# Performance work log

Measured on AMD Instinct MI355X. Metric: run time of the kernel, lower is better.

The kernel has to match this reference:

```python
import jax, jax.numpy as jnp
import numpy as np

D = 256        # feature dim
H = 8          # num_heads
HD = D // H    # head dim = 32
G = 16         # graphs in batch
NA = 128       # nodes per graph, side A
NB = 128       # nodes per graph, side B


def setup_inputs() -> dict:
    key = jax.random.key(0)
    ks = jax.random.split(key, 7)
    s = 1.0 / np.sqrt(D)
    A = jax.random.normal(ks[0], (G * NA, D), dtype=jnp.float32)
    B = jax.random.normal(ks[1], (G * NB, D), dtype=jnp.float32)
    batch1 = jnp.repeat(jnp.arange(G, dtype=jnp.int64), NA)
    batch2 = jnp.repeat(jnp.arange(G, dtype=jnp.int64), NB)
    W1 = jax.random.normal(ks[2], (D, D), dtype=jnp.float32) * s
    bias1 = jax.random.normal(ks[3], (D,), dtype=jnp.float32) * s
    W2 = jax.random.normal(ks[4], (D, D), dtype=jnp.float32) * s
    bias2 = jax.random.normal(ks[5], (D,), dtype=jnp.float32) * s
    q = jax.random.normal(ks[6], (HD,), dtype=jnp.float32) * s
    return {"A": A, "batch1": batch1, "B": B, "batch2": batch2,
            "W1": W1, "bias1": bias1, "W2": W2, "bias2": bias2, "q": q}


def reference(A, batch1, B, batch2, W1, bias1, W2, bias2, q):
    # equal-size graphs: counts are uniform, so torch.split == reshape
    g = int(np.asarray(batch1)[-1]) + 1
    nA = A.shape[0] // g
    nB = B.shape[0] // g
    x1 = A @ W1.T + bias1            # [g*nA, D]
    x2 = B @ W2.T + bias2            # [g*nB, D]
    # faithful to torch: raw C-order view [nA, D] -> [H, nA, HD]
    x1 = x1.reshape(g, H, nA, HD)    # [g, H, nA, hd]
    x2 = x2.reshape(g, H, nB, HD)    # [g, H, nB, hd]
    # att[g,h,i,j] = sum_k tanh(x1[g,h,i,k] * x2[g,h,j,k]) * q[k]
    att = jnp.einsum('ghijk,k->ghij',
                     jnp.tanh(x1[:, :, :, None, :] * x2[:, :, None, :, :]), q)
    b2a = jax.nn.softmax(att.mean(axis=3), axis=2)   # [g, H, nA]
    a2b = jax.nn.softmax(att.mean(axis=2), axis=2)   # [g, H, nB]
    A_p = jnp.einsum('ghik,ghi->ghk', x1, b2a).reshape(g, D)
    B_p = jnp.einsum('ghjk,ghj->ghk', x2, a2b).reshape(g, D)
    return jnp.concatenate([A_p, B_p], axis=1)       # [g, 2D]
```

## Files before the change

### kernel.cpp

```cpp
#include <hip/hip_runtime.h>

#define C2L2E 2.8853900817779268f
#define LOG2E 1.4426950408889634f

#define WS_X1   0
#define WS_X2   524288
#define WS_RS   1048576
#define WS_CQ   1064960

typedef short bf16x8 __attribute__((ext_vector_type(8)));
typedef float f32x4 __attribute__((ext_vector_type(4)));

__device__ __forceinline__ unsigned short bf16rne(float f) {
    unsigned u = __float_as_uint(f);
    u += 0x7FFF + ((u >> 16) & 1);
    return (unsigned short)(u >> 16);
}
__device__ __forceinline__ float bf16tof(unsigned short h) {
    return __uint_as_float(((unsigned)h) << 16);
}
__device__ __forceinline__ float rfl(float x) {
    return __uint_as_float(__builtin_amdgcn_readfirstlane(__float_as_uint(x)));
}
__device__ __forceinline__ void cvt4(float4 v, ushort4* h, ushort4* l) {
    h->x = bf16rne(v.x); l->x = bf16rne(v.x - bf16tof(h->x));
    h->y = bf16rne(v.y); l->y = bf16rne(v.y - bf16tof(h->y));
    h->z = bf16rne(v.z); l->z = bf16rne(v.z - bf16tof(h->z));
    h->w = bf16rne(v.w); l->w = bf16rne(v.w - bf16tof(h->w));
}

__global__ __launch_bounds__(512) void k01_gemm(
        const float* __restrict__ A, const float* __restrict__ B,
        const float* __restrict__ W1, const float* __restrict__ b1,
        const float* __restrict__ W2, const float* __restrict__ b2,
        float* __restrict__ ws) {
    __shared__ unsigned short AH[2048], AL[2048], WH[2048], WL[2048];
    const int bid = blockIdx.x, tid = threadIdx.x;
    const int mat = bid >> 7, idx = bid & 127;
    const int r0 = (idx >> 2) * 64, c0 = (idx & 3) * 64;
    const float* In = mat ? B : A;
    const float* Wm = mat ? W2 : W1;
    const float* bs = mat ? b2 : b1;
    float* xo = ws + (mat ? WS_X2 : WS_X1);

    const int wv = tid >> 6, lane = tid & 63;
    const int rt = wv & 3;
    const int nt0 = (wv >> 2) * 2;

    const int lr = tid >> 3, k4 = tid & 7;
    const int wofs = (((lr >> 4) * 64 + (lr & 15) + ((k4 >> 1) << 4)) * 8 + (k4 & 1) * 4);

    f32x4 acc[2];
    acc[0] = (f32x4){0.f, 0.f, 0.f, 0.f};
    acc[1] = (f32x4){0.f, 0.f, 0.f, 0.f};

    for (int kt = 0; kt < 8; ++kt) {
        if (kt) __syncthreads();
        {
            float4 va = *(const float4*)(In + (size_t)(r0 + lr) * 256 + kt * 32 + k4 * 4);
            ushort4 h, l; cvt4(va, &h, &l);
            *(ushort4*)(AH + wofs) = h;
            *(ushort4*)(AL + wofs) = l;
            float4 vw = *(const float4*)(Wm + (size_t)(c0 + lr) * 256 + kt * 32 + k4 * 4);
            cvt4(vw, &h, &l);
            *(ushort4*)(WH + wofs) = h;
            *(ushort4*)(WL + wofs) = l;
        }
        __syncthreads();
        {
            bf16x8 ah = *(const bf16x8*)(AH + (rt * 64 + lane) * 8);
            bf16x8 al = *(const bf16x8*)(AL + (rt * 64 + lane) * 8);
            #pragma unroll
            for (int nt = 0; nt < 2; ++nt) {
                const int ct = nt0 + nt;
                bf16x8 wh = *(const bf16x8*)(WH + (ct * 64 + lane) * 8);
                bf16x8 wl = *(const bf16x8*)(WL + (ct * 64 + lane) * 8);
                acc[nt] = __builtin_amdgcn_mfma_f32_16x16x32_bf16(ah, wh, acc[nt], 0, 0, 0);
                acc[nt] = __builtin_amdgcn_mfma_f32_16x16x32_bf16(ah, wl, acc[nt], 0, 0, 0);
                acc[nt] = __builtin_amdgcn_mfma_f32_16x16x32_bf16(al, wh, acc[nt], 0, 0, 0);
            }
        }
    }

    const int rowb = r0 + rt * 16 + (lane >> 4) * 4;
    const int l16 = lane & 15;
    #pragma unroll
    for (int nt = 0; nt < 2; ++nt) {
        const int col = c0 + (nt0 + nt) * 16 + l16;
        const float bb = bs[col];
        #pragma unroll
        for (int rg = 0; rg < 4; ++rg)
            xo[(size_t)(rowb + rg) * 256 + col] = acc[nt][rg] + bb;
    }
}

__global__ __launch_bounds__(512, 6) void k2_att(
        const float* __restrict__ x1v, const float* __restrict__ x2v,
        const float* __restrict__ q,
        float* __restrict__ rowsum, float* __restrict__ colq) {
    const int bid = blockIdx.x;
    const int gh = bid >> 2;
    const int qd = bid & 3;
    const int tid = threadIdx.x;
    const int j = tid & 127;
    const int iset = __builtin_amdgcn_readfirstlane(tid >> 7);

    __shared__ float Smat[32 * 132];
    __shared__ float colp[4][128];
    __shared__ float red8[32][8];

    float xr[32];
    {
        const float4* xp = (const float4*)(x2v + (size_t)gh * 4096 + (size_t)j * 32);
        #pragma unroll
        for (int k4 = 0; k4 < 8; ++k4) {
            float4 v = xp[k4];
            xr[k4*4+0] = v.x * C2L2E; xr[k4*4+1] = v.y * C2L2E;
            xr[k4*4+2] = v.z * C2L2E; xr[k4*4+3] = v.w * C2L2E;
        }
    }
    float qt[32];
    #pragma unroll
    for (int k4 = 0; k4 < 8; ++k4) {
        float4 v = *(const float4*)(q + k4 * 4);
        qt[k4*4+0] = rfl(v.x) * -2.0f;
        qt[k4*4+1] = rfl(v.y) * -2.0f;
        qt[k4*4+2] = rfl(v.z) * -2.0f;
        qt[k4*4+3] = rfl(v.w) * -2.0f;
    }

    const float* x1base = x1v + (size_t)gh * 4096 + (size_t)(qd * 32 + iset * 8) * 32;
    float colacc = 0.f;

    for (int r = 0; r < 8; ++r) {
        float a[32];
        #pragma unroll
        for (int k4 = 0; k4 < 8; ++k4) {
            float4 v = *(const float4*)(x1base + r * 32 + k4 * 4);
            a[k4*4+0] = rfl(v.x);
            a[k4*4+1] = rfl(v.y);
            a[k4*4+2] = rfl(v.z);
            a[k4*4+3] = rfl(v.w);
        }
        float S0 = 0.f, S1 = 0.f;
        #pragma unroll
        for (int kp = 0; kp < 16; ++kp) {
            float p0 = a[2*kp]   * xr[2*kp];
            float p1 = a[2*kp+1] * xr[2*kp+1];
            float d0 = __builtin_amdgcn_exp2f(fminf(p0, 60.f)) + 1.f;
            float d1 = __builtin_amdgcn_exp2f(fminf(p1, 60.f)) + 1.f;
            float rD = __builtin_amdgcn_rcpf(d0 * d1);
            float U  = fmaf(qt[2*kp+1], d0, qt[2*kp] * d1);
            if (kp & 1) S1 = fmaf(U, rD, S1); else S0 = fmaf(U, rD, S0);
        }
        float S = S0 + S1;
        colacc += S;
        Smat[(iset * 8 + r) * 132 + j] = S;
    }
    colp[iset][j] = colacc;
    __syncthreads();

    if (tid < 256) {
        const int row = tid >> 3, seg = tid & 7;
        const float4* sp = (const float4*)(Smat + row * 132 + seg * 16);
        float4 v0 = sp[0], v1 = sp[1], v2 = sp[2], v3 = sp[3];
        red8[row][seg] = (v0.x+v0.y+v0.z+v0.w) + (v1.x+v1.y+v1.z+v1.w)
                       + (v2.x+v2.y+v2.z+v2.w) + (v3.x+v3.y+v3.z+v3.w);
    }
    __syncthreads();
    if (tid < 32) {
        float s = 0.f;
        #pragma unroll
        for (int m = 0; m < 8; ++m) s += red8[tid][m];
        rowsum[gh * 128 + qd * 32 + tid] = s;
    }
    if (tid < 128) {
        colq[(size_t)bid * 128 + tid] =
            colp[0][tid] + colp[1][tid] + colp[2][tid] + colp[3][tid];
    }
}

__global__ __launch_bounds__(256) void k3_out(
        const float* __restrict__ x1v, const float* __restrict__ x2v,
        const float* __restrict__ rowsum, const float* __restrict__ colq,
        float* __restrict__ out) {
    const int gh = blockIdx.x;
    const int g = gh >> 3, h = gh & 7;
    const int tid = threadIdx.x;
    const int side = tid >> 7;
    const int u = tid & 127;
    const int w2 = (u >> 6) & 1;
    const int lane = tid & 63;

    __shared__ float warr[2][128];
    __shared__ float red[4];
    __shared__ float red2[4];
    __shared__ float part[2][4][32];

    float m;
    if (side == 0) {
        m = rowsum[gh * 128 + u] * 0.0078125f;
    } else {
        m = (colq[(size_t)(gh * 4 + 0) * 128 + u] + colq[(size_t)(gh * 4 + 1) * 128 + u] +
             colq[(size_t)(gh * 4 + 2) * 128 + u] + colq[(size_t)(gh * 4 + 3) * 128 + u]) * 0.0078125f;
    }

    float mx = m;
    #pragma unroll
    for (int s = 32; s >= 1; s >>= 1) mx = fmaxf(mx, __shfl_xor(mx, s));
    if (lane == 0) red[side * 2 + w2] = mx;
    __syncthreads();
    mx = fmaxf(red[side * 2], red[side * 2 + 1]);

    float e = __builtin_amdgcn_exp2f((m - mx) * LOG2E);
    float sm = e;
    #pragma unroll
    for (int s = 32; s >= 1; s >>= 1) sm += __shfl_xor(sm, s);
    if (lane == 0) red2[side * 2 + w2] = sm;
    __syncthreads();
    const float tot = red2[side * 2] + red2[side * 2 + 1];
    warr[side][u] = e * __builtin_amdgcn_rcpf(tot);
    __syncthreads();

    const int k = u & 31, is = u >> 5;
    const float* xt = (side ? x2v : x1v) + (size_t)gh * 4096;
    float p = 0.f;
    #pragma unroll 4
    for (int r = 0; r < 32; ++r)
        p = fmaf(xt[(is * 32 + r) * 32 + k], warr[side][is * 32 + r], p);
    part[side][is][k] = p;
    __syncthreads();
    if (u < 32) {
        float o = part[side][0][u] + part[side][1][u] + part[side][2][u] + part[side][3][u];
        out[(size_t)g * 512 + side * 256 + h * 32 + u] = o;
    }
}

extern "C" void kernel_launch(void* const* d_in, const int* in_sizes, int n_in,
                              void* d_out, int out_size, void* d_ws, size_t ws_size,
                              hipStream_t stream) {
    const float* A  = (const float*)d_in[0];
    const float* B  = (const float*)d_in[2];
    const float* W1 = (const float*)d_in[4];
    const float* b1 = (const float*)d_in[5];
    const float* W2 = (const float*)d_in[6];
    const float* b2 = (const float*)d_in[7];
    const float* q  = (const float*)d_in[8];
    float* ws  = (float*)d_ws;
    float* out = (float*)d_out;

    k01_gemm<<<256, 512, 0, stream>>>(A, B, W1, b1, W2, b2, ws);
    k2_att<<<512, 512, 0, stream>>>(ws + WS_X1, ws + WS_X2, q, ws + WS_RS, ws + WS_CQ);
    k3_out<<<128, 256, 0, stream>>>(ws + WS_X1, ws + WS_X2, ws + WS_RS, ws + WS_CQ, out);
}
```

Before: 37.45 us.

## Fuse softmax/output stage into attention kernel via last-block atomic ticket

Removes the separate k3_out launch. Each (graph, head) group of four attention blocks increments an atomic counter after writing its partial row and column sums, and the last block to arrive computes both softmaxes and the weighted output. The counter is zeroed inside the GEMM kernel. This saves one kernel launch and its dependency gap, at the cost of thread fences, an atomic per block, and extra shared memory in the attention kernel, which may lower occupancy.

```diff
diff --git a/kernel.cpp b/kernel.cpp
--- a/kernel.cpp
+++ b/kernel.cpp
@@ -7,6 +7,7 @@
 #define WS_X2   524288
 #define WS_RS   1048576
 #define WS_CQ   1064960
+#define WS_CNT  1130496
 
 typedef short bf16x8 __attribute__((ext_vector_type(8)));
 typedef float f32x4 __attribute__((ext_vector_type(4)));
@@ -33,9 +34,10 @@
         const float* __restrict__ A, const float* __restrict__ B,
         const float* __restrict__ W1, const float* __restrict__ b1,
         const float* __restrict__ W2, const float* __restrict__ b2,
-        float* __restrict__ ws) {
+        float* __restrict__ ws, int* __restrict__ cnt) {
     __shared__ unsigned short AH[2048], AL[2048], WH[2048], WL[2048];
     const int bid = blockIdx.x, tid = threadIdx.x;
+    if (bid == 0 && tid < 128) cnt[tid] = 0;
     const int mat = bid >> 7, idx = bid & 127;
     const int r0 = (idx >> 2) * 64, c0 = (idx & 3) * 64;
     const float* In = mat ? B : A;
@@ -94,10 +96,11 @@
     }
 }
 
-__global__ __launch_bounds__(512, 6) void k2_att(
+__global__ __launch_bounds__(512, 6) void k2_att_fin(
         const float* __restrict__ x1v, const float* __restrict__ x2v,
-        const float* __restrict__ q,
-        float* __restrict__ rowsum, float* __restrict__ colq) {
+        const float* __restrict__ q, float* __restrict__ rowsum,
+        float* __restrict__ colq, int* __restrict__ cnt,
+        float* __restrict__ out) {
     const int bid = blockIdx.x;
     const int gh = bid >> 2;
     const int qd = bid & 3;
@@ -108,6 +111,11 @@
     __shared__ float Smat[32 * 132];
     __shared__ float colp[4][128];
     __shared__ float red8[32][8];
+    __shared__ int tkt;
+    __shared__ float warr[2][128];
+    __shared__ float redm[4];
+    __shared__ float red2[4];
+    __shared__ float part[2][4][32];
 
     float xr[32];
     {
@@ -178,59 +186,59 @@
         colq[(size_t)bid * 128 + tid] =
             colp[0][tid] + colp[1][tid] + colp[2][tid] + colp[3][tid];
     }
-}
-
-__global__ __launch_bounds__(256) void k3_out(
-        const float* __restrict__ x1v, const float* __restrict__ x2v,
-        const float* __restrict__ rowsum, const float* __restrict__ colq,
-        float* __restrict__ out) {
-    const int gh = blockIdx.x;
+
+    __threadfence();
+    __syncthreads();
+    if (tid == 0) tkt = atomicAdd(&cnt[gh], 1);
+    __syncthreads();
+    if (tkt != 3) return;
+    __threadfence();
+
     const int g = gh >> 3, h = gh & 7;
-    const int tid = threadIdx.x;
     const int side = tid >> 7;
     const int u = tid & 127;
     const int w2 = (u >> 6) & 1;
     const int lane = tid & 63;
 
-    __shared__ float warr[2][128];
-    __shared__ float red[4];
-    __shared__ float red2[4];
-    __shared__ float part[2][4][32];
-
-    float m;
-    if (side == 0) {
-        m = rowsum[gh * 128 + u] * 0.0078125f;
-    } else {
-        m = (colq[(size_t)(gh * 4 + 0) * 128 + u] + colq[(size_t)(gh * 4 + 1) * 128 + u] +
-             colq[(size_t)(gh * 4 + 2) * 128 + u] + colq[(size_t)(gh * 4 + 3) * 128 + u]) * 0.0078125f;
-    }
-
-    float mx = m;
-    #pragma unroll
-    for (int s = 32; s >= 1; s >>= 1) mx = fmaxf(mx, __shfl_xor(mx, s));
-    if (lane == 0) red[side * 2 + w2] = mx;
-    __syncthreads();
-    mx = fmaxf(red[side * 2], red[side * 2 + 1]);
-
-    float e = __builtin_amdgcn_exp2f((m - mx) * LOG2E);
-    float sm = e;
-    #pragma unroll
-    for (int s = 32; s >= 1; s >>= 1) sm += __shfl_xor(sm, s);
-    if (lane == 0) red2[side * 2 + w2] = sm;
-    __syncthreads();
-    const float tot = red2[side * 2] + red2[side * 2 + 1];
-    warr[side][u] = e * __builtin_amdgcn_rcpf(tot);
-    __syncthreads();
-
-    const int k = u & 31, is = u >> 5;
-    const float* xt = (side ? x2v : x1v) + (size_t)gh * 4096;
-    float p = 0.f;
-    #pragma unroll 4
-    for (int r = 0; r < 32; ++r)
-        p = fmaf(xt[(is * 32 + r) * 32 + k], warr[side][is * 32 + r], p);
-    part[side][is][k] = p;
-    __syncthreads();
-    if (u < 32) {
+    float m = 0.f, e = 0.f;
+    if (tid < 256) {
+        if (side == 0) {
+            m = rowsum[gh * 128 + u] * 0.0078125f;
+        } else {
+            m = (colq[(size_t)(gh * 4 + 0) * 128 + u] + colq[(size_t)(gh * 4 + 1) * 128 + u] +
+                 colq[(size_t)(gh * 4 + 2) * 128 + u] + colq[(size_t)(gh * 4 + 3) * 128 + u]) * 0.0078125f;
+        }
+        float mx = m;
+        #pragma unroll
+        for (int s = 32; s >= 1; s >>= 1) mx = fmaxf(mx, __shfl_xor(mx, s));
+        if (lane == 0) redm[side * 2 + w2] = mx;
+    }
+    __syncthreads();
+    if (tid < 256) {
+        float mx = fmaxf(redm[side * 2], redm[side * 2 + 1]);
+        e = __builtin_amdgcn_exp2f((m - mx) * LOG2E);
+        float sm = e;
+        #pragma unroll
+        for (int s = 32; s >= 1; s >>= 1) sm += __shfl_xor(sm, s);
+        if (lane == 0) red2[side * 2 + w2] = sm;
+    }
+    __syncthreads();
+    if (tid < 256) {
+        const float tot = red2[side * 2] + red2[side * 2 + 1];
+        warr[side][u] = e * __builtin_amdgcn_rcpf(tot);
+    }
+    __syncthreads();
+    if (tid < 256) {
+        const int k = u & 31, is = u >> 5;
+        const float* xt = (side ? x2v : x1v) + (size_t)gh * 4096;
+        float p = 0.f;
+        #pragma unroll 4
+        for (int r = 0; r < 32; ++r)
+            p = fmaf(xt[(is * 32 + r) * 32 + k], warr[side][is * 32 + r], p);
+        part[side][is][k] = p;
+    }
+    __syncthreads();
+    if (tid < 256 && u < 32) {
         float o = part[side][0][u] + part[side][1][u] + part[side][2][u] + part[side][3][u];
         out[(size_t)g * 512 + side * 256 + h * 32 + u] = o;
     }
@@ -248,8 +256,9 @@
     const float* q  = (const float*)d_in[8];
     float* ws  = (float*)d_ws;
     float* out = (float*)d_out;
-
-    k01_gemm<<<256, 512, 0, stream>>>(A, B, W1, b1, W2, b2, ws);
-    k2_att<<<512, 512, 0, stream>>>(ws + WS_X1, ws + WS_X2, q, ws + WS_RS, ws + WS_CQ);
-    k3_out<<<128, 256, 0, stream>>>(ws + WS_X1, ws + WS_X2, ws + WS_RS, ws + WS_CQ, out);
-}
+    int* cnt = (int*)(ws + WS_CNT);
+
+    k01_gemm<<<256, 512, 0, stream>>>(A, B, W1, b1, W2, b2, ws, cnt);
+    k2_att_fin<<<512, 512, 0, stream>>>(ws + WS_X1, ws + WS_X2, q,
+                                        ws + WS_RS, ws + WS_CQ, cnt, out);
+}
```

Result: slower. 147.4 us, median of 2 (+293.6%).
